# Performance work log

Measured on AMD Instinct MI355X. Metric: run time of the kernel, lower is better.

The kernel has to match this reference:

```python
import jax, jax.numpy as jnp
import numpy as np

# dims: batch, dim_d, dim_k, in_ch, out_ch, length, kernel, pad, num segments
B, D, K, CI, CO, L, NB, P, S = 4, 32, 8, 2, 2, 4096, 15, 7, 8


def _segment_ids():
    # replicate PartiallyUnsharedConv1d.repeat_lengths logic
    padded = L + 2 * P
    rough = padded // S
    reps, tot = [], 0
    for i in range(S):
        r = (L - tot) if i == S - 1 else (rough - 2 * P)
        reps.append(r)
        tot += r
    return np.repeat(np.arange(S), reps)  # shape [L]


def setup_inputs() -> dict:
    key = jax.random.key(0)
    k1, k2, k3 = jax.random.split(key, 3)
    x = jax.random.normal(k1, (B, D, K, CI, L), dtype=jnp.float32)
    weight = 0.02 * jax.random.normal(k2, (D, K, CO, CI, S, 1, NB), dtype=jnp.float32)
    bias = 0.02 * jax.random.normal(k3, (D, K, CO, S, 1), dtype=jnp.float32)
    return {"x": x, "weight": weight, "bias": bias}


def reference(x, weight, bias):
    seg = jnp.asarray(_segment_ids())  # [L] segment id per output position
    # zero pad last dim (ConstantPad1d)
    xp = jnp.pad(x, ((0, 0), (0, 0), (0, 0), (0, 0), (P, P)))
    # unfold: sliding windows of size NB, stride 1 -> [b, d, k, i, L, NB]
    idx = jnp.arange(L)[:, None] + jnp.arange(NB)[None, :]
    xu = xp[..., idx]
    # gather per-position segment weights instead of python repeat/cat
    w = weight[:, :, :, :, seg, 0, :]  # [d, k, o, i, L, NB]
    out = jnp.einsum('dkoilf,bdkilf->bdkol', w, xu)  # [b, d, k, o, L]
    out = out + bias[:, :, :, seg, 0]  # bias broadcast over batch
    return out
```

## Files before the change

### kernel.cpp

```cpp
#include <hip/hip_runtime.h>
#include <stdint.h>

constexpr int Bc  = 4;
constexpr int Dc  = 32;
constexpr int Kc  = 8;
constexpr int CIc = 2;
constexpr int COc = 2;
constexpr int Lc  = 4096;
constexpr int NBc = 15;
constexpr int Sc  = 8;

constexpr int NTHREADS = 256;
constexpr int JT       = 4;
constexpr int TILE     = NTHREADS * JT;
constexpr int NTILES   = Lc / TILE;
constexpr int WELEMS   = COc * CIc * Sc * NBc;

typedef float f32x4 __attribute__((ext_vector_type(4)));
typedef const __attribute__((address_space(1))) float* gas1_t;
typedef __attribute__((address_space(3))) float* las3_t;

__device__ __forceinline__ int seg_of(int l) {
    int s = l / 499;
    return s > 7 ? 7 : s;
}

__global__ __launch_bounds__(NTHREADS) void cde_bcr_kernel(
    const float* __restrict__ x,
    const float* __restrict__ w,
    const float* __restrict__ bias,
    float* __restrict__ out)
{
    __shared__ __align__(16) float xs[CIc][Lc + 16];
    __shared__ __align__(16) float wl[COc * CIc * Sc][16];
    __shared__ float bl[COc * Sc];

    const int tid  = threadIdx.x;
    const int lane = tid & 63;
    const int wid  = tid >> 6;
    const int bdk  = blockIdx.x;
    const int dk   = bdk % (Dc * Kc);

    for (int t = tid; t < WELEMS; t += NTHREADS)
        wl[t / NBc][t % NBc] = w[(size_t)dk * WELEMS + t];
    if (tid < COc * Sc)
        bl[tid] = bias[(size_t)dk * (COc * Sc) + tid];
    if (tid < 2 * 16) {
        int i = tid >> 4, e = tid & 15;
        int idx = (e < 8) ? e : (Lc + e);
        xs[i][idx] = 0.0f;
    }
    __builtin_amdgcn_sched_barrier(0);

    const float* xrow = x + (size_t)bdk * CIc * Lc;
#pragma unroll
    for (int q = 0; q < 4; ++q) {
#pragma unroll
        for (int i = 0; i < CIc; ++i) {
            const float* g = xrow + (size_t)i * Lc + q * 1024 + wid * 256 + lane * 4;
            float* lp = &xs[i][8 + q * 1024 + wid * 256];
            __builtin_amdgcn_global_load_lds((gas1_t)g, (las3_t)lp, 16, 0, 0);
        }
    }
    __builtin_amdgcn_sched_barrier(0);

#pragma unroll
    for (int t = 0; t < NTILES; ++t) {
        if (t == 0) {
            asm volatile("s_waitcnt vmcnt(4) lgkmcnt(0)" ::: "memory");
            __builtin_amdgcn_s_barrier();
        } else if (t == 1 || t == 2) {
            asm volatile("s_waitcnt vmcnt(4)" ::: "memory");
            __builtin_amdgcn_s_barrier();
        }

        const int gl0 = t * TILE + tid * JT;
        const int s0  = seg_of(gl0);
        const int s3  = seg_of(gl0 + JT - 1);

        float xa0[20], xa1[20];
#pragma unroll
        for (int m = 0; m < 5; ++m) {
            *(f32x4*)&xa0[4 * m] = *(const f32x4*)&xs[0][gl0 + 4 * m];
            *(f32x4*)&xa1[4 * m] = *(const f32x4*)&xs[1][gl0 + 4 * m];
        }

        float acc[COc][JT];
#pragma unroll
        for (int o = 0; o < COc; ++o)
#pragma unroll
            for (int j = 0; j < JT; ++j)
                acc[o][j] = bl[o * Sc + s0];

#pragma unroll
        for (int i = 0; i < CIc; ++i) {
            float wa[16], wb[16];
#pragma unroll
            for (int m = 0; m < 4; ++m) {
                *(f32x4*)&wa[4 * m] = *(const f32x4*)&wl[(0 * CIc + i) * Sc + s0][4 * m];
                *(f32x4*)&wb[4 * m] = *(const f32x4*)&wl[(1 * CIc + i) * Sc + s0][4 * m];
            }
#pragma unroll
            for (int f = 0; f < NBc; ++f) {
#pragma unroll
                for (int j = 0; j < JT; ++j) {
                    float xv = (i == 0) ? xa0[j + f + 1] : xa1[j + f + 1];
                    acc[0][j] = fmaf(wa[f], xv, acc[0][j]);
                    acc[1][j] = fmaf(wb[f], xv, acc[1][j]);
                }
            }
        }

        if (s3 != s0) {
            const int jstart = 499 * s3 - gl0;
            const float b0 = bl[0 * Sc + s3];
            const float b1 = bl[1 * Sc + s3];
#pragma unroll
            for (int j = 0; j < JT; ++j) {
                if (j >= jstart) {
                    float a0 = b0, a1 = b1;
#pragma unroll
                    for (int i = 0; i < CIc; ++i) {
#pragma unroll
                        for (int f = 0; f < NBc; ++f) {
                            float xv = (i == 0) ? xa0[j + f + 1] : xa1[j + f + 1];
                            a0 = fmaf(wl[(0 * CIc + i) * Sc + s3][f], xv, a0);
                            a1 = fmaf(wl[(1 * CIc + i) * Sc + s3][f], xv, a1);
                        }
                    }
                    acc[0][j] = a0;
                    acc[1][j] = a1;
                }
            }
        }

        float* ob = out + (size_t)bdk * COc * Lc + gl0;
        f32x4 v0 = { acc[0][0], acc[0][1], acc[0][2], acc[0][3] };
        f32x4 v1 = { acc[1][0], acc[1][1], acc[1][2], acc[1][3] };
        __builtin_nontemporal_store(v0, (f32x4*)(ob));
        __builtin_nontemporal_store(v1, (f32x4*)(ob + Lc));
    }
}

extern "C" void kernel_launch(void* const* d_in, const int* in_sizes, int n_in,
                              void* d_out, int out_size, void* d_ws, size_t ws_size,
                              hipStream_t stream) {
    const float* x    = (const float*)d_in[0];
    const float* w    = (const float*)d_in[1];
    const float* bias = (const float*)d_in[2];
    float* out        = (float*)d_out;

    cde_bcr_kernel<<<dim3(Bc * Dc * Kc), NTHREADS, 0, stream>>>(x, w, bias, out);
}
```

Before: 18.97 us.

## Process two batch rows per 512-thread block sharing the same weights

Each block now handles two (b,d,k) rows that share one weight set (blockIdx and blockIdx+512). That halves the number of blocks and the redundant weight and bias loads into LDS. Both rows are prefetched into a double LDS buffer, and the second row's load overlaps compute on the first. Blocks grow to 512 threads and LDS use roughly doubles, which may cut occupancy, and with fewer blocks there are fewer waves to hide latency.

```diff
diff --git a/kernel.cpp b/kernel.cpp
--- a/kernel.cpp
+++ b/kernel.cpp
@@ -10,10 +10,12 @@
 constexpr int NBc = 15;
 constexpr int Sc  = 8;
 
-constexpr int NTHREADS = 256;
+constexpr int NTHREADS = 512;
 constexpr int JT       = 4;
 constexpr int TILE     = NTHREADS * JT;
 constexpr int NTILES   = Lc / TILE;
+constexpr int NROWS    = Bc * Dc * Kc;
+constexpr int NBLK     = NROWS / 2;
 constexpr int WELEMS   = COc * CIc * Sc * NBc;
 
 typedef float f32x4 __attribute__((ext_vector_type(4)));
@@ -31,114 +33,126 @@
     const float* __restrict__ bias,
     float* __restrict__ out)
 {
-    __shared__ __align__(16) float xs[CIc][Lc + 16];
+    __shared__ __align__(16) float xs[2][CIc][Lc + 16];
     __shared__ __align__(16) float wl[COc * CIc * Sc][16];
     __shared__ float bl[COc * Sc];
 
     const int tid  = threadIdx.x;
     const int lane = tid & 63;
-    const int wid  = tid >> 6;
-    const int bdk  = blockIdx.x;
-    const int dk   = bdk % (Dc * Kc);
+    const int wv   = tid >> 6;
+    const int r0   = blockIdx.x;
+    const int r1   = blockIdx.x + NBLK;
+    const int dk   = r0 % (Dc * Kc);
 
-    for (int t = tid; t < WELEMS; t += NTHREADS)
-        wl[t / NBc][t % NBc] = w[(size_t)dk * WELEMS + t];
+    if (tid < WELEMS)
+        wl[tid / NBc][tid % NBc] = w[(size_t)dk * WELEMS + tid];
     if (tid < COc * Sc)
         bl[tid] = bias[(size_t)dk * (COc * Sc) + tid];
-    if (tid < 2 * 16) {
-        int i = tid >> 4, e = tid & 15;
+    if (tid < 2 * CIc * 16) {
+        int bf = tid >> 5, i = (tid >> 4) & 1, e = tid & 15;
         int idx = (e < 8) ? e : (Lc + e);
-        xs[i][idx] = 0.0f;
+        xs[bf][i][idx] = 0.0f;
     }
     __builtin_amdgcn_sched_barrier(0);
 
-    const float* xrow = x + (size_t)bdk * CIc * Lc;
+    const float* xr0 = x + (size_t)r0 * CIc * Lc;
+    const float* xr1 = x + (size_t)r1 * CIc * Lc;
 #pragma unroll
-    for (int q = 0; q < 4; ++q) {
+    for (int i = 0; i < CIc; ++i)
 #pragma unroll
-        for (int i = 0; i < CIc; ++i) {
-            const float* g = xrow + (size_t)i * Lc + q * 1024 + wid * 256 + lane * 4;
-            float* lp = &xs[i][8 + q * 1024 + wid * 256];
-            __builtin_amdgcn_global_load_lds((gas1_t)g, (las3_t)lp, 16, 0, 0);
+        for (int q = 0; q < 2; ++q) {
+            const float* g = xr0 + (size_t)i * Lc + wv * 512 + q * 256 + lane * 4;
+            __builtin_amdgcn_global_load_lds((gas1_t)g,
+                (las3_t)&xs[0][i][8 + wv * 512 + q * 256], 16, 0, 0);
         }
-    }
+#pragma unroll
+    for (int i = 0; i < CIc; ++i)
+#pragma unroll
+        for (int q = 0; q < 2; ++q) {
+            const float* g = xr1 + (size_t)i * Lc + wv * 512 + q * 256 + lane * 4;
+            __builtin_amdgcn_global_load_lds((gas1_t)g,
+                (las3_t)&xs[1][i][8 + wv * 512 + q * 256], 16, 0, 0);
+        }
     __builtin_amdgcn_sched_barrier(0);
 
 #pragma unroll
-    for (int t = 0; t < NTILES; ++t) {
-        if (t == 0) {
-            asm volatile("s_waitcnt vmcnt(4) lgkmcnt(0)" ::: "memory");
-            __builtin_amdgcn_s_barrier();
-        } else if (t == 1 || t == 2) {
-            asm volatile("s_waitcnt vmcnt(4)" ::: "memory");
-            __builtin_amdgcn_s_barrier();
-        }
+    for (int r = 0; r < 2; ++r) {
+        asm volatile("s_waitcnt vmcnt(4) lgkmcnt(0)" ::: "memory");
+        __builtin_amdgcn_s_barrier();
+        __builtin_amdgcn_sched_barrier(0);
 
-        const int gl0 = t * TILE + tid * JT;
-        const int s0  = seg_of(gl0);
-        const int s3  = seg_of(gl0 + JT - 1);
-
-        float xa0[20], xa1[20];
-#pragma unroll
-        for (int m = 0; m < 5; ++m) {
-            *(f32x4*)&xa0[4 * m] = *(const f32x4*)&xs[0][gl0 + 4 * m];
-            *(f32x4*)&xa1[4 * m] = *(const f32x4*)&xs[1][gl0 + 4 * m];
-        }
-
-        float acc[COc][JT];
-#pragma unroll
-        for (int o = 0; o < COc; ++o)
-#pragma unroll
-            for (int j = 0; j < JT; ++j)
-                acc[o][j] = bl[o * Sc + s0];
+        const int row = (r == 0) ? r0 : r1;
+        const float (*xsb)[Lc + 16] = xs[r];
+        float* obase = out + (size_t)row * COc * Lc;
 
 #pragma unroll
-        for (int i = 0; i < CIc; ++i) {
-            float wa[16], wb[16];
+        for (int t = 0; t < NTILES; ++t) {
+            const int gl0 = t * TILE + tid * JT;
+            const int s0  = seg_of(gl0);
+            const int s3  = seg_of(gl0 + JT - 1);
+
+            float xa0[20], xa1[20];
 #pragma unroll
-            for (int m = 0; m < 4; ++m) {
-                *(f32x4*)&wa[4 * m] = *(const f32x4*)&wl[(0 * CIc + i) * Sc + s0][4 * m];
-                *(f32x4*)&wb[4 * m] = *(const f32x4*)&wl[(1 * CIc + i) * Sc + s0][4 * m];
+            for (int m = 0; m < 5; ++m) {
+                *(f32x4*)&xa0[4 * m] = *(const f32x4*)&xsb[0][gl0 + 4 * m];
+                *(f32x4*)&xa1[4 * m] = *(const f32x4*)&xsb[1][gl0 + 4 * m];
             }
+
+            float acc[COc][JT];
 #pragma unroll
-            for (int f = 0; f < NBc; ++f) {
+            for (int o = 0; o < COc; ++o)
+#pragma unroll
+                for (int j = 0; j < JT; ++j)
+                    acc[o][j] = bl[o * Sc + s0];
+
+#pragma unroll
+            for (int i = 0; i < CIc; ++i) {
+                float wa[16], wb[16];
+#pragma unroll
+                for (int m = 0; m < 4; ++m) {
+                    *(f32x4*)&wa[4 * m] = *(const f32x4*)&wl[(0 * CIc + i) * Sc + s0][4 * m];
+                    *(f32x4*)&wb[4 * m] = *(const f32x4*)&wl[(1 * CIc + i) * Sc + s0][4 * m];
+                }
+#pragma unroll
+                for (int f = 0; f < NBc; ++f) {
+#pragma unroll
+                    for (int j = 0; j < JT; ++j) {
+                        float xv = (i == 0) ? xa0[j + f + 1] : xa1[j + f + 1];
+                        acc[0][j] = fmaf(wa[f], xv, acc[0][j]);
+                        acc[1][j] = fmaf(wb[f], xv, acc[1][j]);
+                    }
+                }
+            }
+
+            if (s3 != s0) {
+                const int jstart = 499 * s3 - gl0;
+                const float b0 = bl[0 * Sc + s3];
+                const float b1 = bl[1 * Sc + s3];
 #pragma unroll
                 for (int j = 0; j < JT; ++j) {
-                    float xv = (i == 0) ? xa0[j + f + 1] : xa1[j + f + 1];
-                    acc[0][j] = fmaf(wa[f], xv, acc[0][j]);
-                    acc[1][j] = fmaf(wb[f], xv, acc[1][j]);
+                    if (j >= jstart) {
+                        float a0 = b0, a1 = b1;
+#pragma unroll
+                        for (int i = 0; i < CIc; ++i) {
+#pragma unroll
+                            for (int f = 0; f < NBc; ++f) {
+                                float xv = (i == 0) ? xa0[j + f + 1] : xa1[j + f + 1];
+                                a0 = fmaf(wl[(0 * CIc + i) * Sc + s3][f], xv, a0);
+                                a1 = fmaf(wl[(1 * CIc + i) * Sc + s3][f], xv, a1);
+                            }
+                        }
+                        acc[0][j] = a0;
+                        acc[1][j] = a1;
+                    }
                 }
             }
+
+            float* ob = obase + gl0;
+            f32x4 v0 = { acc[0][0], acc[0][1], acc[0][2], acc[0][3] };
+            f32x4 v1 = { acc[1][0], acc[1][1], acc[1][2], acc[1][3] };
+            __builtin_nontemporal_store(v0, (f32x4*)(ob));
+            __builtin_nontemporal_store(v1, (f32x4*)(ob + Lc));
         }
-
-        if (s3 != s0) {
-            const int jstart = 499 * s3 - gl0;
-            const float b0 = bl[0 * Sc + s3];
-            const float b1 = bl[1 * Sc + s3];
-#pragma unroll
-            for (int j = 0; j < JT; ++j) {
-                if (j >= jstart) {
-                    float a0 = b0, a1 = b1;
-#pragma unroll
-                    for (int i = 0; i < CIc; ++i) {
-#pragma unroll
-                        for (int f = 0; f < NBc; ++f) {
-                            float xv = (i == 0) ? xa0[j + f + 1] : xa1[j + f + 1];
-                            a0 = fmaf(wl[(0 * CIc + i) * Sc + s3][f], xv, a0);
-                            a1 = fmaf(wl[(1 * CIc + i) * Sc + s3][f], xv, a1);
-                        }
-                    }
-                    acc[0][j] = a0;
-                    acc[1][j] = a1;
-                }
-            }
-        }
-
-        float* ob = out + (size_t)bdk * COc * Lc + gl0;
-        f32x4 v0 = { acc[0][0], acc[0][1], acc[0][2], acc[0][3] };
-        f32x4 v1 = { acc[1][0], acc[1][1], acc[1][2], acc[1][3] };
-        __builtin_nontemporal_store(v0, (f32x4*)(ob));
-        __builtin_nontemporal_store(v1, (f32x4*)(ob + Lc));
     }
 }
 
@@ -150,5 +164,5 @@
     const float* bias = (const float*)d_in[2];
     float* out        = (float*)d_out;
 
-    cde_bcr_kernel<<<dim3(Bc * Dc * Kc), NTHREADS, 0, stream>>>(x, w, bias, out);
+    cde_bcr_kernel<<<dim3(NBLK), NTHREADS, 0, stream>>>(x, w, bias, out);
 }
```

New measurement: 19.36 us. +2.0%, slower.
